# Kernel optimization log

Hardware: AMD Instinct MI355X
Metric: run time of the kernel (lower is better)

## Reference

```python
import jax, jax.numpy as jnp
import numpy as np

VOCAB = 32000
EMBED = 1024
HIDDEN = 1024
BATCH = 256
SEQ = 1024


def setup_inputs() -> dict:
    key = jax.random.key(0)
    k1, k2, k3, k4, k5, k6 = jax.random.split(key, 6)
    x = jax.random.randint(k1, (BATCH, SEQ), 0, VOCAB)
    emb = jax.random.normal(k2, (VOCAB, EMBED), dtype=jnp.float32) * 0.02
    # nn.Linear(input_dim, hidden_dim): weight [out, in], bias [out]
    Wi = jax.random.normal(k3, (HIDDEN, EMBED), dtype=jnp.float32) * (1.0 / np.sqrt(EMBED))
    bi = jax.random.normal(k4, (HIDDEN,), dtype=jnp.float32) * 0.01
    Wh = jax.random.normal(k5, (HIDDEN, HIDDEN), dtype=jnp.float32) * (1.0 / np.sqrt(HIDDEN))
    bh = jax.random.normal(k6, (HIDDEN,), dtype=jnp.float32) * 0.01
    return {"x": x, "emb": emb, "Wi": Wi, "bi": bi, "Wh": Wh, "bh": bh}


def reference(x, emb, Wi, bi, Wh, bh):
    # Embed all tokens up front: [B, T, E]
    ex = emb[x]
    # Precompute input projection for every step (batched GEMM): [B, T, H]
    xi = jnp.einsum('bte,he->bth', ex, Wi) + bi
    h0 = jnp.zeros((x.shape[0], Wh.shape[0]), dtype=emb.dtype)

    def step(h, xi_t):  # xi_t: [B, H]
        h_new = jnp.tanh(xi_t + h @ Wh.T + bh)
        return h_new, None

    h_final, _ = jax.lax.scan(step, h0, jnp.swapaxes(xi, 0, 1))  # scan over T
    return h_final  # [B, H]
```

## Files before the change

### kernel.cpp

```cpp
#include <hip/hip_runtime.h>
#include <cmath>

#define BATCHN 256
#define SEQT   1024
#define EMBED  1024
#define HID    1024
#define VOCABN 32000

typedef __attribute__((ext_vector_type(8))) _Float16 half8;
typedef __attribute__((ext_vector_type(4))) _Float16 half4;
typedef __attribute__((ext_vector_type(4))) float    float4v;
typedef __attribute__((ext_vector_type(4))) unsigned int uint4v;

#define LOSCALE 4096.0f
#define LOINV   (1.0f/4096.0f)

union FU16 { _Float16 f; unsigned short u; };
__device__ inline unsigned short f16bits(_Float16 f){ FU16 t; t.f=f; return t.u; }
__device__ inline _Float16 bits16(unsigned short u){ FU16 t; t.u=u; return t.f; }

__device__ inline void async16(const void* g, void* l) {
  __builtin_amdgcn_global_load_lds(
      (const __attribute__((address_space(1))) void*)g,
      (__attribute__((address_space(3))) void*)l, 16, 0, 0);
}

__global__ void convert_f32_f16(const float* __restrict__ in,
                                _Float16* __restrict__ out, int n) {
  int i = (blockIdx.x * blockDim.x + threadIdx.x) * 4;
  if (i + 3 < n) {
    float4v v = *reinterpret_cast<const float4v*>(in + i);
    half4 o;
#pragma unroll
    for (int j = 0; j < 4; ++j) o[j] = (_Float16)v[j];
    *reinterpret_cast<half4*>(out + i) = o;
  }
}

__global__ void split_f32_f16(const float* __restrict__ in,
                              _Float16* __restrict__ hi,
                              _Float16* __restrict__ lo, int n) {
  int i = (blockIdx.x * blockDim.x + threadIdx.x) * 4;
  if (i + 3 < n) {
    float4v v = *reinterpret_cast<const float4v*>(in + i);
    half4 h, l;
#pragma unroll
    for (int j = 0; j < 4; ++j) {
      h[j] = (_Float16)v[j];
      l[j] = (_Float16)((v[j] - (float)h[j]) * LOSCALE);
    }
    *reinterpret_cast<half4*>(hi + i) = h;
    *reinterpret_cast<half4*>(lo + i) = l;
  }
}

__global__ __launch_bounds__(256, 2) void gemm_xi(
    const _Float16* __restrict__ embh,
    const _Float16* __restrict__ Wih,
    const int* __restrict__ x,
    const float* __restrict__ bi,
    _Float16* __restrict__ xi,
    int t0, int Tc)
{
  __shared__ __align__(16) _Float16 As[128 * 64];
  __shared__ __align__(16) _Float16 Bs[128 * 64];
  __shared__ __align__(16) _Float16 stage[128 * 132];
  __shared__ int toks[128];

  const int tid  = threadIdx.x;
  const int wid  = tid >> 6, lane = tid & 63;
  const int nt   = blockIdx.x & 7, mt = blockIdx.x >> 3;
  const int m0   = mt * 128, n0 = nt * 128;

  if (tid < 128) {
    int m  = m0 + tid;
    int tl = m >> 8;
    int b  = m & 255;
    toks[tid] = x[b * SEQT + t0 + tl];
  }
  __syncthreads();

  const _Float16* aptr[4];
  const _Float16* bptr[4];
  int ldsoff[4];
#pragma unroll
  for (int i = 0; i < 4; ++i) {
    int idx = i * 256 + tid;
    int row = idx >> 3, kc = idx & 7;
    aptr[i]   = embh + (size_t)toks[row] * 1024 + kc * 8;
    bptr[i]   = Wih + ((size_t)(n0 + row) << 10) + kc * 8;
    ldsoff[i] = idx * 8;
  }

  float4v acc[4][4] = {};
  const int wm = wid & 1, wn = wid >> 1;
  const int cn = lane & 15, kg = lane >> 4;

  for (int k0 = 0; k0 < 1024; k0 += 64) {
#pragma unroll
    for (int i = 0; i < 4; ++i) {
      async16(aptr[i] + k0, &As[ldsoff[i]]);
      async16(bptr[i] + k0, &Bs[ldsoff[i]]);
    }
    __syncthreads();

    half8 a[4][2], b[4][2];
#pragma unroll
    for (int mf = 0; mf < 4; ++mf)
#pragma unroll
      for (int kf = 0; kf < 2; ++kf)
        a[mf][kf] = *reinterpret_cast<const half8*>(
            &As[(wm * 64 + mf * 16 + cn) * 64 + kf * 32 + kg * 8]);
#pragma unroll
    for (int nf = 0; nf < 4; ++nf)
#pragma unroll
      for (int kf = 0; kf < 2; ++kf)
        b[nf][kf] = *reinterpret_cast<const half8*>(
            &Bs[(wn * 64 + nf * 16 + cn) * 64 + kf * 32 + kg * 8]);

#pragma unroll
    for (int mf = 0; mf < 4; ++mf)
#pragma unroll
      for (int nf = 0; nf < 4; ++nf)
#pragma unroll
        for (int kf = 0; kf < 2; ++kf)
          acc[mf][nf] = __builtin_amdgcn_mfma_f32_16x16x32_f16(
              a[mf][kf], b[nf][kf], acc[mf][nf], 0, 0, 0);
    __syncthreads();
  }

#pragma unroll
  for (int nf = 0; nf < 4; ++nf) {
    int n = wn * 64 + nf * 16 + cn;
    float biv = bi[n0 + n];
#pragma unroll
    for (int mf = 0; mf < 4; ++mf) {
#pragma unroll
      for (int j = 0; j < 4; ++j) {
        int m = wm * 64 + mf * 16 + kg * 4 + j;
        stage[m * 132 + n] = (_Float16)(acc[mf][nf][j] + biv);
      }
    }
  }
  __syncthreads();
#pragma unroll
  for (int p = 0; p < 8; ++p) {
    int chunk = p * 256 + tid;
    int r = chunk >> 4, cc = chunk & 15;
    half4 v0 = *reinterpret_cast<const half4*>(stage + r * 132 + cc * 8);
    half4 v1 = *reinterpret_cast<const half4*>(stage + r * 132 + cc * 8 + 4);
    half8 o;
#pragma unroll
    for (int e = 0; e < 4; ++e) { o[e] = v0[e]; o[4 + e] = v1[e]; }
    int m  = m0 + r;
    int tt = m >> 8, b = m & 255;
    int n  = n0 + cc * 8;
    size_t addr = ((size_t)(tt * 256 + (b >> 4) * 16 + (n >> 6)) << 10)
                + (size_t)((b & 15) * 64 + (n & 63));
    *reinterpret_cast<half8*>(xi + addr) = o;
  }
}

__global__ __launch_bounds__(256, 1) void rnn_scan(
    const _Float16* __restrict__ Whig,
    const _Float16* __restrict__ Wlog,
    const float* __restrict__ bh,
    const _Float16* __restrict__ xi,
    float* __restrict__ hstate,
    float* __restrict__ out,
    _Float16* __restrict__ hexHiA,
    _Float16* __restrict__ hexLoA,
    _Float16* __restrict__ hexHiB,
    _Float16* __restrict__ hexLoB,
    int* __restrict__ bar,
    int t0, int Tc)
{
  __shared__ __align__(16) _Float16 Ahi[16 * 1024];
  __shared__ __align__(16) _Float16 Alo[16 * 1024];

  const int tid  = threadIdx.x;
  const int wv   = tid >> 6, lane = tid & 63;
  const int cn   = lane & 15, kg = lane >> 4;
  const int gb   = blockIdx.x >> 4;
  const int gc   = blockIdx.x & 15;
  const int r0   = gb * 16;
  const int wcol = gc * 64 + wv * 16 + cn;

  half8 whi[32], wlo[32];
  {
    const _Float16* wp = Whig + ((size_t)wcol << 10) + kg * 8;
    const _Float16* lp = Wlog + ((size_t)wcol << 10) + kg * 8;
#pragma unroll
    for (int kk = 0; kk < 32; ++kk) {
      whi[kk] = *reinterpret_cast<const half8*>(wp + kk * 32);
      wlo[kk] = *reinterpret_cast<const half8*>(lp + kk * 32);
    }
  }
  const float bhv = bh[wcol];

  const size_t xibase = ((size_t)(gb * 16 + gc) << 10) + wv * 16 + cn;

  if (t0 == 0) {
#pragma unroll
    for (int p = 0; p < 8; ++p) {
      int idx = p * 256 + tid, row = idx >> 7, cc = idx & 127;
      int bo = (((row << 11) + cc * 16) ^ ((row & 7) << 4));
      half8 z = {0, 0, 0, 0, 0, 0, 0, 0};
      *reinterpret_cast<half8*>(reinterpret_cast<char*>(Ahi) + bo) = z;
      *reinterpret_cast<half8*>(reinterpret_cast<char*>(Alo) + bo) = z;
    }
  } else {
#pragma unroll
    for (int p = 0; p < 8; ++p) {
      int idx = p * 256 + tid, row = idx >> 7, cc = idx & 127;
      const float* hp = hstate + (((size_t)(r0 + row)) << 10) + cc * 8;
      half8 vh, vl;
#pragma unroll
      for (int e = 0; e < 8; ++e) {
        float f = hp[e];
        _Float16 hi = (_Float16)f;
        vh[e] = hi;
        vl[e] = (_Float16)((f - (float)hi) * LOSCALE);
      }
      int bo = (((row << 11) + cc * 16) ^ ((row & 7) << 4));
      *reinterpret_cast<half8*>(reinterpret_cast<char*>(Ahi) + bo) = vh;
      *reinterpret_cast<half8*>(reinterpret_cast<char*>(Alo) + bo) = vl;
    }
  }
  __syncthreads();

  unsigned int xr[4];
#pragma unroll
  for (int j = 0; j < 4; ++j) {
    unsigned long long ap = (unsigned long long)(xi + xibase + (size_t)(kg * 4 + j) * 64);
    asm volatile("global_load_ushort %0, %1, off" : "=v"(xr[j]) : "v"(ap) : "memory");
  }

  uint4v uhi[4], ulo[4];

  for (int tt = 0; tt < Tc; ++tt) {
    float4v a1a = {}, a1b = {}, a2a = {}, a2b = {}, a3a = {}, a3b = {};

#pragma unroll
    for (int kk = 0; kk < 16; ++kk) {
      int ab = (((cn << 11) + kk * 64 + kg * 16) ^ ((cn & 7) << 4));
      half8 ah = *reinterpret_cast<const half8*>(reinterpret_cast<const char*>(Ahi) + ab);
      half8 al = *reinterpret_cast<const half8*>(reinterpret_cast<const char*>(Alo) + ab);
      if (kk & 1) {
        asm("v_mfma_f32_16x16x32_f16 %0, %1, %2, %0" : "+v"(a1b) : "v"(ah), "a"(whi[kk]));
        asm("v_mfma_f32_16x16x32_f16 %0, %1, %2, %0" : "+v"(a2b) : "v"(al), "a"(whi[kk]));
        asm("v_mfma_f32_16x16x32_f16 %0, %1, %2, %0" : "+v"(a3b) : "v"(ah), "a"(wlo[kk]));
      } else {
        asm("v_mfma_f32_16x16x32_f16 %0, %1, %2, %0" : "+v"(a1a) : "v"(ah), "a"(whi[kk]));
        asm("v_mfma_f32_16x16x32_f16 %0, %1, %2, %0" : "+v"(a2a) : "v"(al), "a"(whi[kk]));
        asm("v_mfma_f32_16x16x32_f16 %0, %1, %2, %0" : "+v"(a3a) : "v"(ah), "a"(wlo[kk]));
      }
    }

    if (tt != 0) {
      asm volatile("s_waitcnt vmcnt(0)" ::: "memory");
      __builtin_amdgcn_sched_barrier(0);
#pragma unroll
      for (int p = 0; p < 4; ++p) {
        int c = 1024 + p * 256 + tid;
        int gcb = c >> 7, rowl = (c >> 3) & 15, c8 = c & 7;
        int bo = (((rowl << 11) + gcb * 128 + c8 * 16) ^ ((rowl & 7) << 4));
        *reinterpret_cast<uint4v*>(reinterpret_cast<char*>(Ahi) + bo) = uhi[p];
        *reinterpret_cast<uint4v*>(reinterpret_cast<char*>(Alo) + bo) = ulo[p];
      }
      asm volatile("s_waitcnt lgkmcnt(0)" ::: "memory");
      __builtin_amdgcn_sched_barrier(0);
      __builtin_amdgcn_s_barrier();
    }

#pragma unroll
    for (int kk = 16; kk < 32; ++kk) {
      int ab = (((cn << 11) + kk * 64 + kg * 16) ^ ((cn & 7) << 4));
      half8 ah = *reinterpret_cast<const half8*>(reinterpret_cast<const char*>(Ahi) + ab);
      half8 al = *reinterpret_cast<const half8*>(reinterpret_cast<const char*>(Alo) + ab);
      if (kk & 1) {
        asm("v_mfma_f32_16x16x32_f16 %0, %1, %2, %0" : "+v"(a1b) : "v"(ah), "a"(whi[kk]));
        asm("v_mfma_f32_16x16x32_f16 %0, %1, %2, %0" : "+v"(a2b) : "v"(al), "a"(whi[kk]));
        asm("v_mfma_f32_16x16x32_f16 %0, %1, %2, %0" : "+v"(a3b) : "v"(ah), "a"(wlo[kk]));
      } else {
        asm("v_mfma_f32_16x16x32_f16 %0, %1, %2, %0" : "+v"(a1a) : "v"(ah), "a"(whi[kk]));
        asm("v_mfma_f32_16x16x32_f16 %0, %1, %2, %0" : "+v"(a2a) : "v"(al), "a"(whi[kk]));
        asm("v_mfma_f32_16x16x32_f16 %0, %1, %2, %0" : "+v"(a3a) : "v"(ah), "a"(wlo[kk]));
      }
    }
    asm volatile("s_nop 7\n\ts_nop 7");
    asm volatile("s_waitcnt vmcnt(0)" ::: "memory");

    const int tglob = t0 + tt;
    const int par = (tt + 1) & 1;
    _Float16* WHi = par ? hexHiA : hexHiB;
    _Float16* WLo = par ? hexLoA : hexLoB;
#pragma unroll
    for (int j = 0; j < 4; ++j) {
      int rowl = kg * 4 + j;
      int row  = r0 + rowl;
      float v = (a1a[j] + a1b[j]) +
                (a2a[j] + a2b[j] + a3a[j] + a3b[j]) * LOINV +
                bhv + (float)bits16((unsigned short)xr[j]);
      float ex = __expf(2.0f * v);
      float h  = 1.0f - 2.0f / (ex + 1.0f);
      if (tt < Tc - 1) {
        FU16 thi, tlo;
        thi.f = (_Float16)h;
        tlo.f = (_Float16)((h - (float)thi.f) * LOSCALE);
        size_t off = (((size_t)(gb * 16 + gc)) << 10) + rowl * 64 + wv * 16 + cn;
        asm volatile("global_store_short %0, %1, off sc0 sc1"
                     :: "v"((unsigned long long)(WHi + off)), "v"((unsigned int)thi.u) : "memory");
        asm volatile("global_store_short %0, %1, off sc0 sc1"
                     :: "v"((unsigned long long)(WLo + off)), "v"((unsigned int)tlo.u) : "memory");
      }
      if (tglob == SEQT - 1) out[(((size_t)row) << 10) + wcol] = h;
      else if (tt == Tc - 1) hstate[(((size_t)row) << 10) + wcol] = h;
    }
    if (tt == Tc - 1) break;

    asm volatile("s_waitcnt vmcnt(0)" ::: "memory");
    __builtin_amdgcn_s_barrier();
    const int target = tt + 1;
    if (tid == 0)
      asm volatile("global_store_dword %0, %1, off sc0 sc1"
                   :: "v"((unsigned long long)(bar + (gb * 16 + gc) * 32)),
                      "v"(target) : "memory");

#pragma unroll
    for (int j = 0; j < 4; ++j) {
      unsigned long long ap = (unsigned long long)
          (xi + xibase + (((size_t)(tt + 1)) << 18) + (size_t)(kg * 4 + j) * 64);
      asm volatile("global_load_ushort %0, %1, off" : "=v"(xr[j]) : "v"(ap) : "memory");
    }

    if (tid < 16) {
      const int* fp = bar + (gb * 16 + tid) * 32;
      for (;;) {
        int v;
        asm volatile("global_load_dword %0, %1, off sc0 sc1\n\t"
                     "s_waitcnt vmcnt(0)"
                     : "=v"(v) : "v"((unsigned long long)fp) : "memory");
        if (v >= target) break;
        __builtin_amdgcn_s_sleep(1);
      }
    }
    __builtin_amdgcn_s_barrier();

    const _Float16* SHi = par ? hexHiA : hexHiB;
    const _Float16* SLo = par ? hexLoA : hexLoB;
    uint4v thi0[4], tlo0[4];
#pragma unroll
    for (int p = 0; p < 4; ++p) {
      int c = p * 256 + tid;
      int gcb = c >> 7, rowl = (c >> 3) & 15, c8 = c & 7;
      size_t off = (((size_t)(gb * 16 + gcb)) << 10) + rowl * 64 + c8 * 8;
      asm volatile("global_load_dwordx4 %0, %1, off sc0 sc1"
                   : "=v"(thi0[p]) : "v"((unsigned long long)(SHi + off)) : "memory");
      asm volatile("global_load_dwordx4 %0, %1, off sc0 sc1"
                   : "=v"(tlo0[p]) : "v"((unsigned long long)(SLo + off)) : "memory");
    }
#pragma unroll
    for (int p = 0; p < 4; ++p) {
      int c = 1024 + p * 256 + tid;
      int gcb = c >> 7, rowl = (c >> 3) & 15, c8 = c & 7;
      size_t off = (((size_t)(gb * 16 + gcb)) << 10) + rowl * 64 + c8 * 8;
      asm volatile("global_load_dwordx4 %0, %1, off sc0 sc1"
                   : "=v"(uhi[p]) : "v"((unsigned long long)(SHi + off)) : "memory");
      asm volatile("global_load_dwordx4 %0, %1, off sc0 sc1"
                   : "=v"(ulo[p]) : "v"((unsigned long long)(SLo + off)) : "memory");
    }
    asm volatile("s_waitcnt vmcnt(8)" ::: "memory");
    __builtin_amdgcn_sched_barrier(0);
#pragma unroll
    for (int p = 0; p < 4; ++p) {
      int c = p * 256 + tid;
      int gcb = c >> 7, rowl = (c >> 3) & 15, c8 = c & 7;
      int bo = (((rowl << 11) + gcb * 128 + c8 * 16) ^ ((rowl & 7) << 4));
      *reinterpret_cast<uint4v*>(reinterpret_cast<char*>(Ahi) + bo) = thi0[p];
      *reinterpret_cast<uint4v*>(reinterpret_cast<char*>(Alo) + bo) = tlo0[p];
    }
    asm volatile("s_waitcnt lgkmcnt(0)" ::: "memory");
    __builtin_amdgcn_sched_barrier(0);
    __builtin_amdgcn_s_barrier();
  }
}

extern "C" void kernel_launch(void* const* d_in, const int* in_sizes, int n_in,
                              void* d_out, int out_size, void* d_ws, size_t ws_size,
                              hipStream_t stream) {
  const int*   x   = (const int*)  d_in[0];
  const float* emb = (const float*)d_in[1];
  const float* Wi  = (const float*)d_in[2];
  const float* bi  = (const float*)d_in[3];
  const float* Wh  = (const float*)d_in[4];
  const float* bh  = (const float*)d_in[5];
  float* out = (float*)d_out;

  char* ws = (char*)d_ws;
  size_t off = 0;
  auto alloc = [&](size_t bytes) -> void* {
    void* p = ws + off;
    off = (off + bytes + 255) & ~(size_t)255;
    return p;
  };

  _Float16* embh   = (_Float16*)alloc((size_t)VOCABN * EMBED * 2);
  _Float16* Wih    = (_Float16*)alloc((size_t)HID * EMBED * 2);
  _Float16* Whih   = (_Float16*)alloc((size_t)HID * HID * 2);
  _Float16* Wloh   = (_Float16*)alloc((size_t)HID * HID * 2);
  float*    hstate = (float*)   alloc((size_t)BATCHN * HID * 4);
  _Float16* hexHiA = (_Float16*)alloc((size_t)BATCHN * HID * 2);
  _Float16* hexLoA = (_Float16*)alloc((size_t)BATCHN * HID * 2);
  _Float16* hexHiB = (_Float16*)alloc((size_t)BATCHN * HID * 2);
  _Float16* hexLoB = (_Float16*)alloc((size_t)BATCHN * HID * 2);
  int* bar  = (int*)alloc(256 * 32 * 4);
  size_t fixed = off;

  int Tc = 1024;
  while (Tc > 4 && fixed + (size_t)BATCHN * Tc * HID * 2 > ws_size) Tc >>= 1;
  _Float16* xih = (_Float16*)alloc((size_t)BATCHN * Tc * HID * 2);

  {
    int n = VOCABN * EMBED;
    convert_f32_f16<<<n / 1024, 256, 0, stream>>>(emb, embh, n);
    n = HID * EMBED;
    convert_f32_f16<<<n / 1024, 256, 0, stream>>>(Wi, Wih, n);
    n = HID * HID;
    split_f32_f16<<<n / 1024, 256, 0, stream>>>(Wh, Whih, Wloh, n);
  }

  for (int t0 = 0; t0 < SEQT; t0 += Tc) {
    int grid = (BATCHN * Tc / 128) * 8;
    gemm_xi<<<grid, 256, 0, stream>>>(embh, Wih, x, bi, xih, t0, Tc);
    hipMemsetAsync(bar, 0, 256 * 32 * 4, stream);
    rnn_scan<<<256, 256, 0, stream>>>(Whih, Wloh, bh, xih, hstate, out,
                                      hexHiA, hexLoA, hexHiB, hexLoB, bar, t0, Tc);
  }
}
```

Measured before the change: 5.167 ms.

## Split recurrent GEMM over K across waves with LDS partial-sum reduction

Each wave now owns a quarter of the K dimension for all 64 output columns of the block, instead of a 16-column slice over the full K. Each wave loads only its own K-slice of the exchanged hidden state into LDS. That removes the block-wide barriers between the LDS fill and the MFMA loop, and gives 12 independent accumulator chains instead of 6. The cost is a per-step LDS partial-sum buffer and a __syncthreads reduction before the tanh epilogue.

```diff
diff --git a/kernel.cpp b/kernel.cpp
--- a/kernel.cpp
+++ b/kernel.cpp
@@ -177,6 +177,7 @@
 {
   __shared__ __align__(16) _Float16 Ahi[16 * 1024];
   __shared__ __align__(16) _Float16 Alo[16 * 1024];
+  __shared__ __align__(16) float    part[4 * 64 * 20];
 
   const int tid  = threadIdx.x;
   const int wv   = tid >> 6, lane = tid & 63;
@@ -187,15 +188,15 @@
   const int wcol = gc * 64 + wv * 16 + cn;
 
   half8 whi[32], wlo[32];
-  {
-    const _Float16* wp = Whig + ((size_t)wcol << 10) + kg * 8;
-    const _Float16* lp = Wlog + ((size_t)wcol << 10) + kg * 8;
-#pragma unroll
-    for (int kk = 0; kk < 32; ++kk) {
-      whi[kk] = *reinterpret_cast<const half8*>(wp + kk * 32);
-      wlo[kk] = *reinterpret_cast<const half8*>(lp + kk * 32);
-    }
-  }
+#pragma unroll
+  for (int c = 0; c < 4; ++c)
+#pragma unroll
+    for (int kkl = 0; kkl < 8; ++kkl) {
+      int col = gc * 64 + c * 16 + cn;
+      int k   = (wv * 8 + kkl) * 32 + kg * 8;
+      whi[c * 8 + kkl] = *reinterpret_cast<const half8*>(Whig + ((size_t)col << 10) + k);
+      wlo[c * 8 + kkl] = *reinterpret_cast<const half8*>(Wlog + ((size_t)col << 10) + k);
+    }
   const float bhv = bh[wcol];
 
   const size_t xibase = ((size_t)(gb * 16 + gc) << 10) + wv * 16 + cn;
@@ -236,59 +237,64 @@
     asm volatile("global_load_ushort %0, %1, off" : "=v"(xr[j]) : "v"(ap) : "memory");
   }
 
-  uint4v uhi[4], ulo[4];
+  uint4v u1h[4], u1l[4];
+
+#define MFMA_Q(K0, K1)                                                          \
+  _Pragma("unroll")                                                             \
+  for (int kkl = (K0); kkl < (K1); ++kkl) {                                     \
+    int ab = (((cn << 11) + (wv * 8 + kkl) * 64 + kg * 16) ^ ((cn & 7) << 4));  \
+    half8 ah = *reinterpret_cast<const half8*>(reinterpret_cast<const char*>(Ahi) + ab); \
+    half8 al = *reinterpret_cast<const half8*>(reinterpret_cast<const char*>(Alo) + ab); \
+    _Pragma("unroll")                                                           \
+    for (int c = 0; c < 4; ++c) {                                               \
+      asm("v_mfma_f32_16x16x32_f16 %0, %1, %2, %0" : "+v"(ac1[c]) : "v"(ah), "a"(whi[c * 8 + kkl])); \
+      asm("v_mfma_f32_16x16x32_f16 %0, %1, %2, %0" : "+v"(ac2[c]) : "v"(al), "a"(whi[c * 8 + kkl])); \
+      asm("v_mfma_f32_16x16x32_f16 %0, %1, %2, %0" : "+v"(ac3[c]) : "v"(ah), "a"(wlo[c * 8 + kkl])); \
+    }                                                                           \
+  }
 
   for (int tt = 0; tt < Tc; ++tt) {
-    float4v a1a = {}, a1b = {}, a2a = {}, a2b = {}, a3a = {}, a3b = {};
-
-#pragma unroll
-    for (int kk = 0; kk < 16; ++kk) {
-      int ab = (((cn << 11) + kk * 64 + kg * 16) ^ ((cn & 7) << 4));
-      half8 ah = *reinterpret_cast<const half8*>(reinterpret_cast<const char*>(Ahi) + ab);
-      half8 al = *reinterpret_cast<const half8*>(reinterpret_cast<const char*>(Alo) + ab);
-      if (kk & 1) {
-        asm("v_mfma_f32_16x16x32_f16 %0, %1, %2, %0" : "+v"(a1b) : "v"(ah), "a"(whi[kk]));
-        asm("v_mfma_f32_16x16x32_f16 %0, %1, %2, %0" : "+v"(a2b) : "v"(al), "a"(whi[kk]));
-        asm("v_mfma_f32_16x16x32_f16 %0, %1, %2, %0" : "+v"(a3b) : "v"(ah), "a"(wlo[kk]));
-      } else {
-        asm("v_mfma_f32_16x16x32_f16 %0, %1, %2, %0" : "+v"(a1a) : "v"(ah), "a"(whi[kk]));
-        asm("v_mfma_f32_16x16x32_f16 %0, %1, %2, %0" : "+v"(a2a) : "v"(al), "a"(whi[kk]));
-        asm("v_mfma_f32_16x16x32_f16 %0, %1, %2, %0" : "+v"(a3a) : "v"(ah), "a"(wlo[kk]));
-      }
-    }
+    float4v ac1[4] = {}, ac2[4] = {}, ac3[4] = {};
+
+    MFMA_Q(0, 4)
 
     if (tt != 0) {
       asm volatile("s_waitcnt vmcnt(0)" ::: "memory");
       __builtin_amdgcn_sched_barrier(0);
 #pragma unroll
       for (int p = 0; p < 4; ++p) {
-        int c = 1024 + p * 256 + tid;
-        int gcb = c >> 7, rowl = (c >> 3) & 15, c8 = c & 7;
+        int gcbl = 2 + (p >> 1), ch = (p & 1) * 64 + lane;
+        int rowl = ch >> 3, c8 = ch & 7;
+        int gcb  = wv * 4 + gcbl;
         int bo = (((rowl << 11) + gcb * 128 + c8 * 16) ^ ((rowl & 7) << 4));
-        *reinterpret_cast<uint4v*>(reinterpret_cast<char*>(Ahi) + bo) = uhi[p];
-        *reinterpret_cast<uint4v*>(reinterpret_cast<char*>(Alo) + bo) = ulo[p];
+        *reinterpret_cast<uint4v*>(reinterpret_cast<char*>(Ahi) + bo) = u1h[p];
+        *reinterpret_cast<uint4v*>(reinterpret_cast<char*>(Alo) + bo) = u1l[p];
       }
       asm volatile("s_waitcnt lgkmcnt(0)" ::: "memory");
       __builtin_amdgcn_sched_barrier(0);
-      __builtin_amdgcn_s_barrier();
-    }
-
-#pragma unroll
-    for (int kk = 16; kk < 32; ++kk) {
-      int ab = (((cn << 11) + kk * 64 + kg * 16) ^ ((cn & 7) << 4));
-      half8 ah = *reinterpret_cast<const half8*>(reinterpret_cast<const char*>(Ahi) + ab);
-      half8 al = *reinterpret_cast<const half8*>(reinterpret_cast<const char*>(Alo) + ab);
-      if (kk & 1) {
-        asm("v_mfma_f32_16x16x32_f16 %0, %1, %2, %0" : "+v"(a1b) : "v"(ah), "a"(whi[kk]));
-        asm("v_mfma_f32_16x16x32_f16 %0, %1, %2, %0" : "+v"(a2b) : "v"(al), "a"(whi[kk]));
-        asm("v_mfma_f32_16x16x32_f16 %0, %1, %2, %0" : "+v"(a3b) : "v"(ah), "a"(wlo[kk]));
-      } else {
-        asm("v_mfma_f32_16x16x32_f16 %0, %1, %2, %0" : "+v"(a1a) : "v"(ah), "a"(whi[kk]));
-        asm("v_mfma_f32_16x16x32_f16 %0, %1, %2, %0" : "+v"(a2a) : "v"(al), "a"(whi[kk]));
-        asm("v_mfma_f32_16x16x32_f16 %0, %1, %2, %0" : "+v"(a3a) : "v"(ah), "a"(wlo[kk]));
-      }
-    }
+    }
+
+    MFMA_Q(4, 8)
     asm volatile("s_nop 7\n\ts_nop 7");
+
+#pragma unroll
+    for (int c = 0; c < 4; ++c) {
+      float4v pv;
+#pragma unroll
+      for (int j = 0; j < 4; ++j)
+        pv[j] = ac1[c][j] + (ac2[c][j] + ac3[c][j]) * LOINV;
+      *reinterpret_cast<float4v*>(&part[(wv * 64 + c * 16 + cn) * 20 + kg * 4]) = pv;
+    }
+    __syncthreads();
+
+    float4v vs = {};
+#pragma unroll
+    for (int w = 0; w < 4; ++w) {
+      float4v pw = *reinterpret_cast<const float4v*>(
+          &part[(w * 64 + wv * 16 + cn) * 20 + kg * 4]);
+#pragma unroll
+      for (int j = 0; j < 4; ++j) vs[j] += pw[j];
+    }
     asm volatile("s_waitcnt vmcnt(0)" ::: "memory");
 
     const int tglob = t0 + tt;
@@ -299,9 +305,7 @@
     for (int j = 0; j < 4; ++j) {
       int rowl = kg * 4 + j;
       int row  = r0 + rowl;
-      float v = (a1a[j] + a1b[j]) +
-                (a2a[j] + a2b[j] + a3a[j] + a3b[j]) * LOINV +
-                bhv + (float)bits16((unsigned short)xr[j]);
+      float v = vs[j] + bhv + (float)bits16((unsigned short)xr[j]);
       float ex = __expf(2.0f * v);
       float h  = 1.0f - 2.0f / (ex + 1.0f);
       if (tt < Tc - 1) {
@@ -349,41 +353,44 @@
 
     const _Float16* SHi = par ? hexHiA : hexHiB;
     const _Float16* SLo = par ? hexLoA : hexLoB;
-    uint4v thi0[4], tlo0[4];
+    uint4v u0h[4], u0l[4];
 #pragma unroll
     for (int p = 0; p < 4; ++p) {
-      int c = p * 256 + tid;
-      int gcb = c >> 7, rowl = (c >> 3) & 15, c8 = c & 7;
+      int gcbl = p >> 1, ch = (p & 1) * 64 + lane;
+      int rowl = ch >> 3, c8 = ch & 7;
+      int gcb  = wv * 4 + gcbl;
       size_t off = (((size_t)(gb * 16 + gcb)) << 10) + rowl * 64 + c8 * 8;
       asm volatile("global_load_dwordx4 %0, %1, off sc0 sc1"
-                   : "=v"(thi0[p]) : "v"((unsigned long long)(SHi + off)) : "memory");
+                   : "=v"(u0h[p]) : "v"((unsigned long long)(SHi + off)) : "memory");
       asm volatile("global_load_dwordx4 %0, %1, off sc0 sc1"
-                   : "=v"(tlo0[p]) : "v"((unsigned long long)(SLo + off)) : "memory");
+                   : "=v"(u0l[p]) : "v"((unsigned long long)(SLo + off)) : "memory");
     }
 #pragma unroll
     for (int p = 0; p < 4; ++p) {
-      int c = 1024 + p * 256 + tid;
-      int gcb = c >> 7, rowl = (c >> 3) & 15, c8 = c & 7;
+      int gcbl = 2 + (p >> 1), ch = (p & 1) * 64 + lane;
+      int rowl = ch >> 3, c8 = ch & 7;
+      int gcb  = wv * 4 + gcbl;
       size_t off = (((size_t)(gb * 16 + gcb)) << 10) + rowl * 64 + c8 * 8;
       asm volatile("global_load_dwordx4 %0, %1, off sc0 sc1"
-                   : "=v"(uhi[p]) : "v"((unsigned long long)(SHi + off)) : "memory");
+                   : "=v"(u1h[p]) : "v"((unsigned long long)(SHi + off)) : "memory");
       asm volatile("global_load_dwordx4 %0, %1, off sc0 sc1"
-                   : "=v"(ulo[p]) : "v"((unsigned long long)(SLo + off)) : "memory");
+                   : "=v"(u1l[p]) : "v"((unsigned long long)(SLo + off)) : "memory");
     }
     asm volatile("s_waitcnt vmcnt(8)" ::: "memory");
     __builtin_amdgcn_sched_barrier(0);
 #pragma unroll
     for (int p = 0; p < 4; ++p) {
-      int c = p * 256 + tid;
-      int gcb = c >> 7, rowl = (c >> 3) & 15, c8 = c & 7;
+      int gcbl = p >> 1, ch = (p & 1) * 64 + lane;
+      int rowl = ch >> 3, c8 = ch & 7;
+      int gcb  = wv * 4 + gcbl;
       int bo = (((rowl << 11) + gcb * 128 + c8 * 16) ^ ((rowl & 7) << 4));
-      *reinterpret_cast<uint4v*>(reinterpret_cast<char*>(Ahi) + bo) = thi0[p];
-      *reinterpret_cast<uint4v*>(reinterpret_cast<char*>(Alo) + bo) = tlo0[p];
+      *reinterpret_cast<uint4v*>(reinterpret_cast<char*>(Ahi) + bo) = u0h[p];
+      *reinterpret_cast<uint4v*>(reinterpret_cast<char*>(Alo) + bo) = u0l[p];
     }
     asm volatile("s_waitcnt lgkmcnt(0)" ::: "memory");
     __builtin_amdgcn_sched_barrier(0);
-    __builtin_amdgcn_s_barrier();
-  }
+  }
+#undef MFMA_Q
 }
 
 extern "C" void kernel_launch(void* const* d_in, const int* in_sizes, int n_in,
```

New measurement: 5.018 ms (median of 2 runs). 1.03x faster.
